# Optimization experiments

Measured on AMD Instinct MI355X. Metric: run time of the kernel, lower is better.

Reference implementation:

```python
import jax, jax.numpy as jnp
import numpy as np

D_MODEL = 1024
N_HEADS = 16
D_K = D_MODEL // N_HEADS
B, L = 4, 2048


def setup_inputs() -> dict:
    key = jax.random.key(0)
    ks = jax.random.split(key, 9)
    s = 1.0 / np.sqrt(D_MODEL)
    return {
        "x": jax.random.normal(ks[0], (B, L, D_MODEL), dtype=jnp.float32),
        "Wq": jax.random.normal(ks[1], (D_MODEL, D_MODEL), dtype=jnp.float32) * s,
        "bq": jax.random.normal(ks[2], (D_MODEL,), dtype=jnp.float32) * 0.01,
        "Wk": jax.random.normal(ks[3], (D_MODEL, D_MODEL), dtype=jnp.float32) * s,
        "bk": jax.random.normal(ks[4], (D_MODEL,), dtype=jnp.float32) * 0.01,
        "Wv": jax.random.normal(ks[5], (D_MODEL, D_MODEL), dtype=jnp.float32) * s,
        "bv": jax.random.normal(ks[6], (D_MODEL,), dtype=jnp.float32) * 0.01,
        "Wo": jax.random.normal(ks[7], (D_MODEL, D_MODEL), dtype=jnp.float32) * s,
        "bo": jax.random.normal(ks[8], (D_MODEL,), dtype=jnp.float32) * 0.01,
    }


def reference(x, Wq, bq, Wk, bk, Wv, bv, Wo, bo):
    b, l, d = x.shape
    scale = jnp.asarray(np.sqrt(D_K), x.dtype)
    # project and split heads: [B, H, L, d_k]
    def heads(w, bias):
        p = x @ w.T + bias
        return p.reshape(b, l, N_HEADS, D_K).transpose(0, 2, 1, 3)
    Q = heads(Wq, bq)
    K = heads(Wk, bk)
    V = heads(Wv, bv)
    scores = jnp.einsum("bhqd,bhkd->bhqk", Q, K) / scale
    scores = jnp.clip(scores, -100.0, 100.0)
    attn = jax.nn.softmax(scores, axis=-1)  # dropout is identity in eval
    ctx = jnp.einsum("bhqk,bhkd->bhqd", attn, V)
    ctx = ctx.transpose(0, 2, 1, 3).reshape(b, l, d)
    return ctx @ Wo.T + bo
```

## Files before the change

### kernel.cpp

```cpp
#include <hip/hip_runtime.h>
#include <stdint.h>

#define L_SEQ   2048
#define DM      1024
#define NH      16
#define DK      64
#define BATCH   4
#define M_TOK   (BATCH * L_SEQ)

typedef __attribute__((ext_vector_type(8))) short bf16x8;
typedef __attribute__((ext_vector_type(4))) float f32x4;
typedef __attribute__((ext_vector_type(16))) float f32x16;
typedef __attribute__((ext_vector_type(4))) unsigned int u32x4;

typedef __attribute__((address_space(1))) void void_g;
typedef __attribute__((address_space(3))) void void_l;

#define EXP2F(x) __builtin_amdgcn_exp2f(x)

__device__ __forceinline__ unsigned short f2bf(float f) {
  unsigned int u = __builtin_bit_cast(unsigned int, f);
  u += 0x7FFFu + ((u >> 16) & 1u);
  return (unsigned short)(u >> 16);
}

__global__ void cvt_f32_bf16(const float* __restrict__ src,
                             unsigned short* __restrict__ dst, int n4) {
  int i = blockIdx.x * blockDim.x + threadIdx.x;
  int stride = gridDim.x * blockDim.x;
  for (; i < n4; i += stride) {
    float4 v = ((const float4*)src)[i];
    ushort4 o;
    o.x = f2bf(v.x); o.y = f2bf(v.y); o.z = f2bf(v.z); o.w = f2bf(v.w);
    ((ushort4*)dst)[i] = o;
  }
}

__global__ void cvt_w4(const float* __restrict__ s0, const float* __restrict__ s1,
                       const float* __restrict__ s2, const float* __restrict__ s3,
                       unsigned short* __restrict__ dst) {
  int i = blockIdx.x * blockDim.x + threadIdx.x;
  int sel = i >> 18, j = i & 0x3FFFF;
  const float* s = sel == 0 ? s0 : sel == 1 ? s1 : sel == 2 ? s2 : s3;
  float4 v = ((const float4*)s)[j];
  ushort4 o;
  o.x = f2bf(v.x); o.y = f2bf(v.y); o.z = f2bf(v.z); o.w = f2bf(v.w);
  ((ushort4*)(dst + (size_t)sel * DM * DM))[j] = o;
}

#define GBM 128
#define GBN 256
#define GBK 64
#define NKT (DM / GBK)
#define ATILE (GBM * GBK)
#define BTILE (GBN * GBK)
#define BUFE (ATILE + BTILE)

__device__ __forceinline__ void stage_A(
    const unsigned short* __restrict__ A, unsigned short* buf,
    int tm, int k0, int t) {
  const int l = t & 63, w = t >> 6;
  const int su = (l & 7) ^ (l >> 3);
  const int rw = w * 8 + (l >> 3);
  const unsigned short* asrc = A + (size_t)(tm + rw) * DM + k0 + su * 8;
#pragma unroll
  for (int r = 0; r < 2; ++r)
    __builtin_amdgcn_global_load_lds(
        (const void_g*)(asrc + (size_t)r * 64 * DM),
        (void_l*)(buf + r * 4096 + w * 512), 16, 0, 0);
}

__device__ __forceinline__ void stage_B(
    const unsigned short* __restrict__ Bw, unsigned short* buf,
    int tn, int k0, int t) {
  const int l = t & 63, w = t >> 6;
  const int su = (l & 7) ^ (l >> 3);
  const int rw = w * 8 + (l >> 3);
  const unsigned short* bsrc = Bw + (size_t)(tn + rw) * DM + k0 + su * 8;
#pragma unroll
  for (int r = 0; r < 4; ++r)
    __builtin_amdgcn_global_load_lds(
        (const void_g*)(bsrc + (size_t)r * 64 * DM),
        (void_l*)(buf + ATILE + r * 4096 + w * 512), 16, 0, 0);
}

__device__ __forceinline__ bf16x8 frag_ld(const unsigned short* base, int R, int u) {
  return *(const bf16x8*)(base + R * 64 + (u ^ (R & 7)) * 8);
}

template <int EPI>
__global__ __launch_bounds__(512, 2) void gemm8(
    const unsigned short* __restrict__ A,
    const unsigned short* __restrict__ Bw,
    const float* __restrict__ b0, const float* __restrict__ b1,
    const float* __restrict__ b2, float qscale,
    void* __restrict__ out) {
  __shared__ unsigned short L[3 * BUFE];

  const int tidx = threadIdx.x;
  const int wid = tidx >> 6, lane = tidx & 63;
  const int wm = wid >> 2, wn = wid & 3;
  const int lr = lane & 15, lg4 = lane >> 4;

  int wg = blockIdx.y * gridDim.x + blockIdx.x;
  int nwg = gridDim.x * gridDim.y;
  int swz = (wg & 7) * (nwg >> 3) + (wg >> 3);
  const int tm = (swz / gridDim.x) * GBM, tn = (swz % gridDim.x) * GBN;

  f32x4 acc[4][4];
#pragma unroll
  for (int m = 0; m < 4; ++m)
#pragma unroll
    for (int n = 0; n < 4; ++n) acc[m][n] = (f32x4)0.0f;

  stage_A(A, L, tm, 0, tidx);
  stage_B(Bw, L, tn, 0, tidx);
  stage_A(A, L + BUFE, tm, GBK, tidx);
  stage_B(Bw, L + BUFE, tn, GBK, tidx);
  asm volatile("s_waitcnt vmcnt(6)" ::: "memory");
  __builtin_amdgcn_s_barrier();

  for (int i = 0; i < NKT; ++i) {
    unsigned short* cb = L + (i % 3) * BUFE;
    unsigned short* nb = L + ((i + 2) % 3) * BUFE;
    const bool pf = (i + 2 < NKT);
    const int kn = (i + 2) * GBK;

    bf16x8 a0[4], bv0[4];
#pragma unroll
    for (int m = 0; m < 4; ++m)
      a0[m] = frag_ld(cb, wm * 64 + m * 16 + lr, lg4);
#pragma unroll
    for (int n = 0; n < 4; ++n)
      bv0[n] = frag_ld(cb + ATILE, wn * 64 + n * 16 + lr, lg4);
    if (pf) stage_A(A, nb, tm, kn, tidx);
    __builtin_amdgcn_s_barrier();
    asm volatile("s_waitcnt lgkmcnt(0)" ::: "memory");
    __builtin_amdgcn_s_setprio(1);
#pragma unroll
    for (int m = 0; m < 4; ++m)
#pragma unroll
      for (int n = 0; n < 4; ++n)
        acc[m][n] = __builtin_amdgcn_mfma_f32_16x16x32_bf16(a0[m], bv0[n], acc[m][n], 0, 0, 0);
    __builtin_amdgcn_s_setprio(0);
    __builtin_amdgcn_s_barrier();

    bf16x8 a1[4], bv1[4];
#pragma unroll
    for (int m = 0; m < 4; ++m)
      a1[m] = frag_ld(cb, wm * 64 + m * 16 + lr, 4 + lg4);
#pragma unroll
    for (int n = 0; n < 4; ++n)
      bv1[n] = frag_ld(cb + ATILE, wn * 64 + n * 16 + lr, 4 + lg4);
    if (pf) {
      stage_B(Bw, nb, tn, kn, tidx);
      asm volatile("s_waitcnt vmcnt(6)" ::: "memory");
    } else {
      asm volatile("s_waitcnt vmcnt(0)" ::: "memory");
    }
    __builtin_amdgcn_s_barrier();
    asm volatile("s_waitcnt lgkmcnt(0)" ::: "memory");
    __builtin_amdgcn_s_setprio(1);
#pragma unroll
    for (int m = 0; m < 4; ++m)
#pragma unroll
      for (int n = 0; n < 4; ++n)
        acc[m][n] = __builtin_amdgcn_mfma_f32_16x16x32_bf16(a1[m], bv1[n], acc[m][n], 0, 0, 0);
    __builtin_amdgcn_s_setprio(0);
    __builtin_amdgcn_s_barrier();
  }

  if (EPI == 1) {
    float* o = (float*)out;
#pragma unroll
    for (int m = 0; m < 4; ++m) {
      int row0 = tm + wm * 64 + m * 16 + lg4 * 4;
#pragma unroll
      for (int n = 0; n < 4; ++n) {
        int col = tn + wn * 64 + n * 16 + lr;
        float bc = b0[col];
#pragma unroll
        for (int jj = 0; jj < 4; ++jj)
          o[(size_t)(row0 + jj) * DM + col] = acc[m][n][jj] + bc;
      }
    }
  } else {
    const int sel = tn >> 10;
    const float* bias = sel == 0 ? b0 : sel == 1 ? b1 : b2;
    const float scl = sel == 0 ? qscale : 1.0f;
    unsigned short* dst = (unsigned short*)out + (size_t)sel * (8u << 20);
    unsigned short* C = L;
    const int bb = tm >> 11, l0 = tm & 2047;
    const int tnl = tn & 1023;

    if (sel < 2) {
#pragma unroll
      for (int m = 0; m < 4; ++m) {
        int row0 = wm * 64 + m * 16 + lg4 * 4;
#pragma unroll
        for (int n = 0; n < 4; ++n) {
          int col = wn * 64 + n * 16 + lr;
          float bc = bias[tnl + col];
#pragma unroll
          for (int jj = 0; jj < 4; ++jj)
            C[(row0 + jj) * 264 + col] = f2bf((acc[m][n][jj] + bc) * scl);
        }
      }
      __syncthreads();
#pragma unroll
      for (int j = 0; j < 8; ++j) {
        int c = j * 512 + tidx;
        int ll = c >> 5, colc = (c & 31) * 8;
        bf16x8 v = *(const bf16x8*)&C[ll * 264 + colc];
        int c10 = tnl + colc;
        int h = c10 >> 6, dd = c10 & 63;
        *(bf16x8*)&dst[(((size_t)bb * NH + h) * L_SEQ + (l0 + ll)) * DK + dd] = v;
      }
    } else {
#pragma unroll
      for (int m = 0; m < 4; ++m) {
        int row0 = wm * 64 + m * 16 + lg4 * 4;
#pragma unroll
        for (int n = 0; n < 4; ++n) {
          int col = wn * 64 + n * 16 + lr;
          float bc = bias[tnl + col];
          ushort4 pk;
          pk.x = f2bf(acc[m][n][0] + bc);
          pk.y = f2bf(acc[m][n][1] + bc);
          pk.z = f2bf(acc[m][n][2] + bc);
          pk.w = f2bf(acc[m][n][3] + bc);
          *(ushort4*)&C[col * 136 + row0] = pk;
        }
      }
      __syncthreads();
#pragma unroll
      for (int j = 0; j < 8; ++j) {
        int c = j * 512 + tidx;
        int ddl = c >> 4, tk = (c & 15) * 8;
        bf16x8 v = *(const bf16x8*)&C[ddl * 136 + tk];
        int c10 = tnl + ddl;
        int h = c10 >> 6, dd = c10 & 63;
        *(bf16x8*)&dst[(((size_t)bb * NH + h) * DK + dd) * L_SEQ + (l0 + tk)] = v;
      }
    }
  }
}

#define KVB 64
#define LDK 68
#define NTILE (L_SEQ / KVB)
#define FIXM  32.0f
#define CLO  (-144.269504f - FIXM)
#define CHI  (144.269504f - FIXM)

__device__ __forceinline__ bf16x8 lds_frag(const unsigned short* p) {
  uint2 a = *(const uint2*)p;
  uint2 b = *(const uint2*)(p + 4);
  u32x4 t = {a.x, a.y, b.x, b.y};
  return __builtin_bit_cast(bf16x8, t);
}

__device__ __forceinline__ void lds_st16(unsigned short* p, uint4 v) {
  *(uint2*)p = make_uint2(v.x, v.y);
  *(uint2*)(p + 4) = make_uint2(v.z, v.w);
}

__device__ __forceinline__ unsigned cvtpk(float a, float b) {
  unsigned r;
  asm("v_cvt_pk_bf16_f32 %0, %1, %2" : "=v"(r) : "v"(a), "v"(b));
  return r;
}

__device__ __forceinline__ void pl32swap(unsigned& a, unsigned& b) {
  unsigned sa = (unsigned)__shfl_xor((int)a, 32);
  unsigned sb = (unsigned)__shfl_xor((int)b, 32);
  int hi = (threadIdx.x & 63) >> 5;
  unsigned na = hi ? sb : a;
  unsigned nb = hi ? b : sa;
  a = na; b = nb;
}

__device__ __forceinline__ void xpair32(float x, float& lo, float& hi2) {
  unsigned a = __builtin_bit_cast(unsigned, x), b = a;
  pl32swap(a, b);
  lo = __builtin_bit_cast(float, a);
  hi2 = __builtin_bit_cast(float, b);
}

#define MFMA32(a, b, c) __builtin_amdgcn_mfma_f32_32x32x16_bf16(a, b, c, 0, 0, 0)

__global__ __launch_bounds__(256, 4) void flash_attn(
    const unsigned short* __restrict__ Qg,
    const unsigned short* __restrict__ Kg,
    const unsigned short* __restrict__ VTg,
    unsigned short* __restrict__ ctx) {
  __shared__ unsigned short Ks[2][64 * LDK];
  __shared__ unsigned short Vs[2][64 * LDK];

  const int bh = blockIdx.x, b = bh >> 4, h = bh & 15;
  const int q0 = blockIdx.y * 128;
  const int tid = threadIdx.x;
  const int w = tid >> 6, lane = tid & 63;
  const int l31 = lane & 31, hi = lane >> 5;
  const size_t head = (size_t)bh * (L_SEQ * DK);

  const int srow = w * 16 + (lane >> 2);
  const int scol = (lane & 3) * 16;

  bf16x8 qf[4];
  {
    const unsigned short* qp = Qg + head + (size_t)(q0 + w * 32 + l31) * DK + hi * 8;
#pragma unroll
    for (int ks = 0; ks < 4; ++ks) qf[ks] = *(const bf16x8*)(qp + ks * 16);
  }

  f32x16 o[2];
  o[0] = (f32x16)0.0f; o[1] = (f32x16)0.0f;
  float lq = 0.0f;

  {
    const unsigned short* kp = Kg + head + (size_t)srow * DK + scol;
    uint4 k0 = *(const uint4*)kp, k1 = *(const uint4*)(kp + 8);
    const unsigned short* vp = VTg + head + (size_t)srow * L_SEQ + scol;
    uint4 v0 = *(const uint4*)vp, v1 = *(const uint4*)(vp + 8);
    lds_st16(Ks[0] + srow * LDK + scol, k0);
    lds_st16(Ks[0] + srow * LDK + scol + 8, k1);
    lds_st16(Vs[0] + srow * LDK + scol, v0);
    lds_st16(Vs[0] + srow * LDK + scol + 8, v1);
  }
  __syncthreads();

  int cur = 0;
  for (int t = 0; t < NTILE; ++t) {
    uint4 kr0, kr1, vr0, vr1;
    const int kv0n = (t + 1) * KVB;
    if (t + 1 < NTILE) {
      const unsigned short* kp = Kg + head + (size_t)(kv0n + srow) * DK + scol;
      kr0 = *(const uint4*)kp; kr1 = *(const uint4*)(kp + 8);
    }

    f32x16 s0 = (f32x16)(-FIXM), s1 = (f32x16)(-FIXM);
#pragma unroll
    for (int ks = 0; ks < 4; ++ks) {
      bf16x8 k0 = lds_frag(Ks[cur] + l31 * LDK + ks * 16 + hi * 8);
      s0 = MFMA32(k0, qf[ks], s0);
      bf16x8 k1 = lds_frag(Ks[cur] + (32 + l31) * LDK + ks * 16 + hi * 8);
      s1 = MFMA32(k1, qf[ks], s1);
    }

    float ls = 0.0f;
#pragma unroll
    for (int r = 0; r < 16; ++r) {
      s0[r] = EXP2F(__builtin_amdgcn_fmed3f(s0[r], CLO, CHI));
      s1[r] = EXP2F(__builtin_amdgcn_fmed3f(s1[r], CLO, CHI));
    }
    {
      float l4[4];
#pragma unroll
      for (int r = 0; r < 4; ++r)
        l4[r] = ((s0[r] + s0[r + 4]) + (s0[r + 8] + s0[r + 12]))
              + ((s1[r] + s1[r + 4]) + (s1[r + 8] + s1[r + 12]));
      ls = (l4[0] + l4[1]) + (l4[2] + l4[3]);
      float a, c; xpair32(ls, a, c);
      lq += a + c;
    }

    bf16x8 pa[4];
#pragma unroll
    for (int ks = 0; ks < 4; ++ks) {
      const int s8 = (ks & 1) * 8;
      const f32x16 sv = (ks < 2) ? s0 : s1;
      unsigned uA0 = cvtpk(sv[s8 + 0], sv[s8 + 1]);
      unsigned uA1 = cvtpk(sv[s8 + 2], sv[s8 + 3]);
      unsigned uB0 = cvtpk(sv[s8 + 4], sv[s8 + 5]);
      unsigned uB1 = cvtpk(sv[s8 + 6], sv[s8 + 7]);
      pl32swap(uA0, uB0);
      pl32swap(uA1, uB1);
      u32x4 tt = {uA0, uA1, uB0, uB1};
      pa[ks] = __builtin_bit_cast(bf16x8, tt);
    }

    if (t + 1 < NTILE) {
      const unsigned short* vp = VTg + head + (size_t)srow * L_SEQ + kv0n + scol;
      vr0 = *(const uint4*)vp; vr1 = *(const uint4*)(vp + 8);
    }

#pragma unroll
    for (int jb = 0; jb < 2; ++jb)
#pragma unroll
      for (int ks = 0; ks < 4; ++ks) {
        bf16x8 vf = lds_frag(Vs[cur] + (32 * jb + l31) * LDK + ks * 16 + hi * 8);
        o[jb] = MFMA32(vf, pa[ks], o[jb]);
      }

    if (t + 1 < NTILE) {
      lds_st16(Ks[cur ^ 1] + srow * LDK + scol, kr0);
      lds_st16(Ks[cur ^ 1] + srow * LDK + scol + 8, kr1);
      lds_st16(Vs[cur ^ 1] + srow * LDK + scol, vr0);
      lds_st16(Vs[cur ^ 1] + srow * LDK + scol + 8, vr1);
    }
    __syncthreads();
    cur ^= 1;
  }

  {
    float inv = 1.0f / lq;
    const int tok = q0 + w * 32 + l31;
    size_t base = ((size_t)b * L_SEQ + tok) * DM + h * DK;
#pragma unroll
    for (int jb = 0; jb < 2; ++jb)
#pragma unroll
      for (int c = 0; c < 4; ++c) {
        ushort4 pk;
        pk.x = f2bf(o[jb][4 * c + 0] * inv);
        pk.y = f2bf(o[jb][4 * c + 1] * inv);
        pk.z = f2bf(o[jb][4 * c + 2] * inv);
        pk.w = f2bf(o[jb][4 * c + 3] * inv);
        *(ushort4*)&ctx[base + jb * 32 + c * 8 + hi * 4] = pk;
      }
  }
}

extern "C" void kernel_launch(void* const* d_in, const int* in_sizes, int n_in,
                              void* d_out, int out_size, void* d_ws, size_t ws_size,
                              hipStream_t stream) {
  (void)in_sizes; (void)n_in; (void)out_size; (void)ws_size;
  const float* x  = (const float*)d_in[0];
  const float* Wq = (const float*)d_in[1];
  const float* bq = (const float*)d_in[2];
  const float* Wk = (const float*)d_in[3];
  const float* bk = (const float*)d_in[4];
  const float* Wv = (const float*)d_in[5];
  const float* bv = (const float*)d_in[6];
  const float* Wo = (const float*)d_in[7];
  const float* bo = (const float*)d_in[8];

  char* ws = (char*)d_ws;
  unsigned short* xb  = (unsigned short*)(ws);
  unsigned short* wqb = (unsigned short*)(ws + (16ull << 20));
  unsigned short* wob = (unsigned short*)(ws + (22ull << 20));
  unsigned short* Qb  = (unsigned short*)(ws + (24ull << 20));
  unsigned short* Kb  = (unsigned short*)(ws + (40ull << 20));
  unsigned short* VTb = (unsigned short*)(ws + (56ull << 20));
  unsigned short* ctx = xb;

  cvt_f32_bf16<<<2048, 256, 0, stream>>>(x, xb, M_TOK * DM / 4);
  cvt_w4<<<4096, 256, 0, stream>>>(Wq, Wk, Wv, Wo, wqb);

  gemm8<0><<<dim3(3 * DM / GBN, M_TOK / GBM), 512, 0, stream>>>(
      xb, wqb, bq, bk, bv, 0.1803368801f, Qb);

  dim3 ga(BATCH * NH, L_SEQ / 128);
  flash_attn<<<ga, 256, 0, stream>>>(Qb, Kb, VTb, ctx);

  gemm8<1><<<dim3(DM / GBN, M_TOK / GBM), 512, 0, stream>>>(
      ctx, wob, bo, nullptr, nullptr, 1.0f, d_out);
}
```

Measured before the change: 200.5 us.

## Shrink GEMM K-tile to 32, single barrier per step, smaller output-proj tile

Rewrites the bf16 GEMM pipeline to use a 32-wide K tile with a new swizzle and a templated staging helper. Each K step now issues both A and B prefetches together and uses one barrier instead of the earlier split half-steps with two barriers each. The output projection switches to a 128x128 tile with 4 waves, giving more workgroups and higher occupancy bounds. The intent is less LDS use per block and fewer barriers, traded against twice as many K iterations and less MFMA work per synchronisation.

```diff
diff --git a/kernel.cpp b/kernel.cpp
--- a/kernel.cpp
+++ b/kernel.cpp
@@ -48,64 +48,51 @@
   ((ushort4*)(dst + (size_t)sel * DM * DM))[j] = o;
 }
 
-#define GBM 128
-#define GBN 256
-#define GBK 64
+#define GBK 32
 #define NKT (DM / GBK)
-#define ATILE (GBM * GBK)
-#define BTILE (GBN * GBK)
-#define BUFE (ATILE + BTILE)
-
-__device__ __forceinline__ void stage_A(
-    const unsigned short* __restrict__ A, unsigned short* buf,
-    int tm, int k0, int t) {
+#define AT32 (128 * GBK)
+
+template <int NW, int NCH>
+__device__ __forceinline__ void stage32(
+    const unsigned short* __restrict__ S, unsigned short* buf,
+    int row0, int k0, int t) {
   const int l = t & 63, w = t >> 6;
-  const int su = (l & 7) ^ (l >> 3);
-  const int rw = w * 8 + (l >> 3);
-  const unsigned short* asrc = A + (size_t)(tm + rw) * DM + k0 + su * 8;
-#pragma unroll
-  for (int r = 0; r < 2; ++r)
+  const int su = (l & 3) ^ ((l >> 3) & 3);
+  const int rl = l >> 2;
+#pragma unroll
+  for (int r = 0; r < NCH / NW; ++r) {
+    const int c = r * NW + w;
     __builtin_amdgcn_global_load_lds(
-        (const void_g*)(asrc + (size_t)r * 64 * DM),
-        (void_l*)(buf + r * 4096 + w * 512), 16, 0, 0);
-}
-
-__device__ __forceinline__ void stage_B(
-    const unsigned short* __restrict__ Bw, unsigned short* buf,
-    int tn, int k0, int t) {
-  const int l = t & 63, w = t >> 6;
-  const int su = (l & 7) ^ (l >> 3);
-  const int rw = w * 8 + (l >> 3);
-  const unsigned short* bsrc = Bw + (size_t)(tn + rw) * DM + k0 + su * 8;
-#pragma unroll
-  for (int r = 0; r < 4; ++r)
-    __builtin_amdgcn_global_load_lds(
-        (const void_g*)(bsrc + (size_t)r * 64 * DM),
-        (void_l*)(buf + ATILE + r * 4096 + w * 512), 16, 0, 0);
-}
-
-__device__ __forceinline__ bf16x8 frag_ld(const unsigned short* base, int R, int u) {
-  return *(const bf16x8*)(base + R * 64 + (u ^ (R & 7)) * 8);
-}
-
-template <int EPI>
-__global__ __launch_bounds__(512, 2) void gemm8(
+        (const void_g*)(S + (size_t)(row0 + c * 16 + rl) * DM + k0 + su * 8),
+        (void_l*)(buf + c * 512), 16, 0, 0);
+  }
+}
+
+__device__ __forceinline__ bf16x8 frag_ld32(const unsigned short* base, int R, int u) {
+  return *(const bf16x8*)(base + R * 32 + ((u ^ ((R >> 1) & 3)) * 8));
+}
+
+template <int EPI, int BN_, int NW>
+__global__ __launch_bounds__(NW * 64, EPI == 0 ? 4 : 3) void gemm8(
     const unsigned short* __restrict__ A,
     const unsigned short* __restrict__ Bw,
     const float* __restrict__ b0, const float* __restrict__ b1,
     const float* __restrict__ b2, float qscale,
     void* __restrict__ out) {
+  constexpr int BUFE = (128 + BN_) * GBK;
+  constexpr int BCH = BN_ / 16;
   __shared__ unsigned short L[3 * BUFE];
 
   const int tidx = threadIdx.x;
   const int wid = tidx >> 6, lane = tidx & 63;
-  const int wm = wid >> 2, wn = wid & 3;
+  constexpr int WN = NW / 2;
+  const int wm = wid / WN, wn = wid % WN;
   const int lr = lane & 15, lg4 = lane >> 4;
 
   int wg = blockIdx.y * gridDim.x + blockIdx.x;
   int nwg = gridDim.x * gridDim.y;
   int swz = (wg & 7) * (nwg >> 3) + (wg >> 3);
-  const int tm = (swz / gridDim.x) * GBM, tn = (swz % gridDim.x) * GBN;
+  const int tm = (swz / gridDim.x) * 128, tn = (swz % gridDim.x) * BN_;
 
   f32x4 acc[4][4];
 #pragma unroll
@@ -113,60 +100,47 @@
 #pragma unroll
     for (int n = 0; n < 4; ++n) acc[m][n] = (f32x4)0.0f;
 
-  stage_A(A, L, tm, 0, tidx);
-  stage_B(Bw, L, tn, 0, tidx);
-  stage_A(A, L + BUFE, tm, GBK, tidx);
-  stage_B(Bw, L + BUFE, tn, GBK, tidx);
-  asm volatile("s_waitcnt vmcnt(6)" ::: "memory");
+  stage32<NW, 8>(A, L, tm, 0, tidx);
+  stage32<NW, BCH>(Bw, L + AT32, tn, 0, tidx);
+  stage32<NW, 8>(A, L + BUFE, tm, GBK, tidx);
+  stage32<NW, BCH>(Bw, L + BUFE + AT32, tn, GBK, tidx);
+  if constexpr (EPI == 0) asm volatile("s_waitcnt vmcnt(3)" ::: "memory");
+  else                    asm volatile("s_waitcnt vmcnt(4)" ::: "memory");
   __builtin_amdgcn_s_barrier();
 
   for (int i = 0; i < NKT; ++i) {
     unsigned short* cb = L + (i % 3) * BUFE;
     unsigned short* nb = L + ((i + 2) % 3) * BUFE;
     const bool pf = (i + 2 < NKT);
-    const int kn = (i + 2) * GBK;
-
-    bf16x8 a0[4], bv0[4];
+
+    bf16x8 a[4], b[4];
 #pragma unroll
     for (int m = 0; m < 4; ++m)
-      a0[m] = frag_ld(cb, wm * 64 + m * 16 + lr, lg4);
+      a[m] = frag_ld32(cb, wm * 64 + m * 16 + lr, lg4);
 #pragma unroll
     for (int n = 0; n < 4; ++n)
-      bv0[n] = frag_ld(cb + ATILE, wn * 64 + n * 16 + lr, lg4);
-    if (pf) stage_A(A, nb, tm, kn, tidx);
-    __builtin_amdgcn_s_barrier();
+      b[n] = frag_ld32(cb + AT32, wn * 64 + n * 16 + lr, lg4);
+
+    if (pf) {
+      stage32<NW, 8>(A, nb, tm, (i + 2) * GBK, tidx);
+      stage32<NW, BCH>(Bw, nb + AT32, tn, (i + 2) * GBK, tidx);
+    }
+
     asm volatile("s_waitcnt lgkmcnt(0)" ::: "memory");
     __builtin_amdgcn_s_setprio(1);
 #pragma unroll
     for (int m = 0; m < 4; ++m)
 #pragma unroll
       for (int n = 0; n < 4; ++n)
-        acc[m][n] = __builtin_amdgcn_mfma_f32_16x16x32_bf16(a0[m], bv0[n], acc[m][n], 0, 0, 0);
+        acc[m][n] = __builtin_amdgcn_mfma_f32_16x16x32_bf16(a[m], b[n], acc[m][n], 0, 0, 0);
     __builtin_amdgcn_s_setprio(0);
-    __builtin_amdgcn_s_barrier();
-
-    bf16x8 a1[4], bv1[4];
-#pragma unroll
-    for (int m = 0; m < 4; ++m)
-      a1[m] = frag_ld(cb, wm * 64 + m * 16 + lr, 4 + lg4);
-#pragma unroll
-    for (int n = 0; n < 4; ++n)
-      bv1[n] = frag_ld(cb + ATILE, wn * 64 + n * 16 + lr, 4 + lg4);
+
     if (pf) {
-      stage_B(Bw, nb, tn, kn, tidx);
-      asm volatile("s_waitcnt vmcnt(6)" ::: "memory");
+      if constexpr (EPI == 0) asm volatile("s_waitcnt vmcnt(3)" ::: "memory");
+      else                    asm volatile("s_waitcnt vmcnt(4)" ::: "memory");
     } else {
       asm volatile("s_waitcnt vmcnt(0)" ::: "memory");
     }
-    __builtin_amdgcn_s_barrier();
-    asm volatile("s_waitcnt lgkmcnt(0)" ::: "memory");
-    __builtin_amdgcn_s_setprio(1);
-#pragma unroll
-    for (int m = 0; m < 4; ++m)
-#pragma unroll
-      for (int n = 0; n < 4; ++n)
-        acc[m][n] = __builtin_amdgcn_mfma_f32_16x16x32_bf16(a1[m], bv1[n], acc[m][n], 0, 0, 0);
-    __builtin_amdgcn_s_setprio(0);
     __builtin_amdgcn_s_barrier();
   }
 
@@ -348,7 +322,6 @@
       s1 = MFMA32(k1, qf[ks], s1);
     }
 
-    float ls = 0.0f;
 #pragma unroll
     for (int r = 0; r < 16; ++r) {
       s0[r] = EXP2F(__builtin_amdgcn_fmed3f(s0[r], CLO, CHI));
@@ -360,7 +333,7 @@
       for (int r = 0; r < 4; ++r)
         l4[r] = ((s0[r] + s0[r + 4]) + (s0[r + 8] + s0[r + 12]))
               + ((s1[r] + s1[r + 4]) + (s1[r + 8] + s1[r + 12]));
-      ls = (l4[0] + l4[1]) + (l4[2] + l4[3]);
+      float ls = (l4[0] + l4[1]) + (l4[2] + l4[3]);
       float a, c; xpair32(ls, a, c);
       lq += a + c;
     }
@@ -447,12 +420,12 @@
   cvt_f32_bf16<<<2048, 256, 0, stream>>>(x, xb, M_TOK * DM / 4);
   cvt_w4<<<4096, 256, 0, stream>>>(Wq, Wk, Wv, Wo, wqb);
 
-  gemm8<0><<<dim3(3 * DM / GBN, M_TOK / GBM), 512, 0, stream>>>(
+  gemm8<0, 256, 8><<<dim3(3 * DM / 256, M_TOK / 128), 512, 0, stream>>>(
       xb, wqb, bq, bk, bv, 0.1803368801f, Qb);
 
   dim3 ga(BATCH * NH, L_SEQ / 128);
   flash_attn<<<ga, 256, 0, stream>>>(Qb, Kb, VTb, ctx);
 
-  gemm8<1><<<dim3(DM / GBN, M_TOK / GBM), 512, 0, stream>>>(
+  gemm8<1, 128, 4><<<dim3(DM / 128, M_TOK / 128), 256, 0, stream>>>(
       ctx, wob, bo, nullptr, nullptr, 1.0f, d_out);
 }
```

Result: faster. 192.0 us (-4.2%).
